# Kernel optimization log

Hardware: AMD Instinct MI355X
Metric: run time of the kernel (lower is better)

The kernel has to match this reference:

```python
import jax, jax.numpy as jnp
import numpy as np

N = 100000      # nodes
K = 16          # fixed degree (num_ngbrs)
E = N * K       # edges
NFEAT = 128
NHID = 64
OPFEAT = 64


def setup_inputs() -> dict:
    key = jax.random.key(0)
    ks = jax.random.split(key, 8)
    x = jax.random.normal(ks[0], (N, NFEAT), dtype=jnp.float32)
    # edges sorted by destination node, exactly K per node (required by the
    # original e.view(-1, num_ngbrs) softmax reshape)
    edge_row = jnp.repeat(jnp.arange(N, dtype=jnp.int32), K)
    edge_col = jax.random.randint(ks[1], (E,), 0, N, dtype=jnp.int32)
    stdv1 = 1.0 / np.sqrt(NHID)
    stdv2 = 1.0 / np.sqrt(OPFEAT)
    W1 = jax.random.uniform(ks[2], (NFEAT, NHID), jnp.float32, -stdv1, stdv1)
    b1 = jax.random.uniform(ks[3], (NHID,), jnp.float32, -stdv1, stdv1)
    a1 = jax.random.normal(ks[4], (2 * NHID,), jnp.float32) * 0.1
    W2 = jax.random.uniform(ks[5], (NHID, OPFEAT), jnp.float32, -stdv2, stdv2)
    b2 = jax.random.uniform(ks[6], (OPFEAT,), jnp.float32, -stdv2, stdv2)
    a2 = jax.random.normal(ks[7], (2 * OPFEAT,), jnp.float32) * 0.1
    return {"x": x, "edge_row": edge_row, "edge_col": edge_col,
            "W1": W1, "a1": a1, "b1": b1, "W2": W2, "a2": a2, "b2": b2,
            "k": K}


def _gat_layer(x, W, a, b, edge_row, edge_col, k):
    n = x.shape[0]
    h = x @ W                                        # [N, F_out]
    # edge score: concat(h[dst], h[src]) . a  -> leaky_relu
    h_edge = jnp.concatenate([h[edge_row], h[edge_col]], axis=1)  # [E, 2F]
    e = jax.nn.leaky_relu(h_edge @ a, negative_slope=0.2)         # [E]
    # per-destination softmax over the fixed K neighbors (edges row-sorted)
    att = jax.nn.softmax(e.reshape(-1, k), axis=1).reshape(-1)    # [E]
    att = jax.lax.stop_gradient(att)  # original detaches attention
    # sparse (adj * attention) @ h  ==  segment-sum of att_e * h[src_e]
    out = jax.ops.segment_sum(att[:, None] * h[edge_col], edge_row,
                              num_segments=n)
    return out + b


def reference(x, edge_row, edge_col, W1, a1, b1, W2, a2, b2, k):
    x1 = jax.nn.relu(_gat_layer(x, W1, a1, b1, edge_row, edge_col, k))
    x2 = jax.nn.relu(_gat_layer(x1, W2, a2, b2, edge_row, edge_col, k))
    return x2
```

## Files before the change

### kernel.cpp

```cpp
#include <hip/hip_runtime.h>


typedef __attribute__((ext_vector_type(8))) _Float16 f16x8;
typedef __attribute__((ext_vector_type(4))) _Float16 f16x4;
typedef __attribute__((ext_vector_type(4))) float floatx4;

__device__ inline float ubitf(unsigned u) { union { unsigned u; float f; } v; v.u = u; return v.f; }
__device__ inline unsigned fbitu(float f) { union { float f; unsigned u; } v; v.f = f; return v.u; }

template<int KD, bool A_F16>
__global__ __launch_bounds__(256, 2) void gemm_score_f16(
    const void* __restrict__ Xv, const float* __restrict__ W,
    const float* __restrict__ av, _Float16* __restrict__ H,
    float* __restrict__ s1, float* __restrict__ s2, int n)
{
    constexpr int NKT = KD / 32;
    constexpr int NF = NKT * 4 * 64;
    __shared__ f16x8 Bhi[NF];
    __shared__ f16x8 Blo[NF];
    const int tid = threadIdx.x;

    for (int f = tid; f < NF; f += 256) {
        const int ln = f & 63, ntk = f >> 6;
        const int kt = ntk >> 2, nt = ntk & 3;
        const int kbase = kt * 32 + (ln >> 4) * 8;
        const int ccol = nt * 16 + (ln & 15);
        f16x8 hh, ll;
#pragma unroll
        for (int j = 0; j < 8; j++) {
            const float w = W[(kbase + j) * 64 + ccol];
            const _Float16 wh = (_Float16)w;
            hh[j] = wh;
            ll[j] = (_Float16)(w - (float)wh);
        }
        Bhi[f] = hh; Blo[f] = ll;
    }
    __syncthreads();

    const int wave = tid >> 6, lane = tid & 63;
    const int quad = lane >> 4, l15 = lane & 15;
    const int r0 = blockIdx.x * 192 + wave * 48;

    float a1c[4], a2c[4];
#pragma unroll
    for (int nt = 0; nt < 4; nt++) {
        a1c[nt] = av[nt * 16 + l15];
        a2c[nt] = av[64 + nt * 16 + l15];
    }

    f16x8 A[NKT][3];
    if constexpr (A_F16) {
        const _Float16* X = (const _Float16*)Xv;
#pragma unroll
        for (int rb = 0; rb < 3; rb++) {
            int ra = r0 + rb * 16 + l15; if (ra > n - 1) ra = n - 1;
            const _Float16* xp = &X[(size_t)ra * KD + quad * 8];
#pragma unroll
            for (int kt = 0; kt < NKT; kt++)
                A[kt][rb] = *(const f16x8*)(xp + kt * 32);
        }
    } else {
        const float* X = (const float*)Xv;
        float4 raw[NKT][3][2];
#pragma unroll
        for (int rb = 0; rb < 3; rb++) {
            int ra = r0 + rb * 16 + l15; if (ra > n - 1) ra = n - 1;
            const float* xp = &X[(size_t)ra * KD + quad * 8];
#pragma unroll
            for (int kt = 0; kt < NKT; kt++) {
                raw[kt][rb][0] = *(const float4*)(xp + kt * 32);
                raw[kt][rb][1] = *(const float4*)(xp + kt * 32 + 4);
            }
        }
#pragma unroll
        for (int kt = 0; kt < NKT; kt++)
#pragma unroll
            for (int rb = 0; rb < 3; rb++) {
                f16x8 a;
                a[0] = (_Float16)raw[kt][rb][0].x; a[1] = (_Float16)raw[kt][rb][0].y;
                a[2] = (_Float16)raw[kt][rb][0].z; a[3] = (_Float16)raw[kt][rb][0].w;
                a[4] = (_Float16)raw[kt][rb][1].x; a[5] = (_Float16)raw[kt][rb][1].y;
                a[6] = (_Float16)raw[kt][rb][1].z; a[7] = (_Float16)raw[kt][rb][1].w;
                A[kt][rb] = a;
            }
    }

    floatx4 acc[4][3];
#pragma unroll
    for (int nt = 0; nt < 4; nt++)
#pragma unroll
        for (int rb = 0; rb < 3; rb++) acc[nt][rb] = (floatx4){0, 0, 0, 0};

#pragma unroll
    for (int kt = 0; kt < NKT; kt++) {
#pragma unroll
        for (int nt = 0; nt < 4; nt++) {
            const f16x8 bh = Bhi[(kt * 4 + nt) * 64 + lane];
            const f16x8 bl = Blo[(kt * 4 + nt) * 64 + lane];
#pragma unroll
            for (int rb = 0; rb < 3; rb++) {
                acc[nt][rb] = __builtin_amdgcn_mfma_f32_16x16x32_f16(A[kt][rb], bh, acc[nt][rb], 0, 0, 0);
                acc[nt][rb] = __builtin_amdgcn_mfma_f32_16x16x32_f16(A[kt][rb], bl, acc[nt][rb], 0, 0, 0);
            }
        }
    }

#pragma unroll
    for (int rb = 0; rb < 3; rb++) {
        float p1[4] = {0, 0, 0, 0}, p2[4] = {0, 0, 0, 0};
#pragma unroll
        for (int nt = 0; nt < 4; nt++) {
#pragma unroll
            for (int reg = 0; reg < 4; reg++) {
                const int r = r0 + rb * 16 + quad * 4 + reg;
                if (r < n) H[(size_t)r * 64 + nt * 16 + l15] = (_Float16)acc[nt][rb][reg];
                p1[reg] = fmaf(acc[nt][rb][reg], a1c[nt], p1[reg]);
                p2[reg] = fmaf(acc[nt][rb][reg], a2c[nt], p2[reg]);
            }
        }
#pragma unroll
        for (int m = 1; m < 16; m <<= 1) {
#pragma unroll
            for (int reg = 0; reg < 4; reg++) {
                p1[reg] += __shfl_xor(p1[reg], m, 64);
                p2[reg] += __shfl_xor(p2[reg], m, 64);
            }
        }
        if (l15 == 0) {
#pragma unroll
            for (int reg = 0; reg < 4; reg++) {
                const int r = r0 + rb * 16 + quad * 4 + reg;
                if (r < n) { s1[r] = p1[reg]; s2[r] = p2[reg]; }
            }
        }
    }
}

template<typename OT>
__global__ __launch_bounds__(512) void attn_agg(
    const _Float16* __restrict__ H, const float* __restrict__ s1,
    const float* __restrict__ s2, const int* __restrict__ col,
    const float* __restrict__ bias, OT* __restrict__ out, int n)
{
    const int lane = threadIdx.x & 63;
    const int wv = threadIdx.x >> 6;
    const int j = lane & 15;
    const int dst = blockIdx.x * 32 + wv * 4 + (lane >> 4);
    if (dst >= n) return;

    const int c = col[dst * 16 + j];
    float e = s1[dst] + s2[c];
    e = (e > 0.0f) ? e : 0.2f * e;
    float m = e;
#pragma unroll
    for (int mk = 1; mk < 16; mk <<= 1) m = fmaxf(m, __shfl_xor(m, mk, 64));
    float p = __expf(e - m);
    float s = p;
#pragma unroll
    for (int mk = 1; mk < 16; mk <<= 1) s += __shfl_xor(s, mk, 64);
    const float att = p / s;

    const int bbase = (lane & 48) << 2;
    int srck[16]; float attk[16];
#pragma unroll
    for (int k = 0; k < 16; k++) {
        const int bidx = bbase + (k << 2);
        srck[k] = __builtin_amdgcn_ds_bpermute(bidx, c);
        attk[k] = ubitf((unsigned)__builtin_amdgcn_ds_bpermute(bidx, (int)fbitu(att)));
    }
    f16x4 hv[16];
#pragma unroll
    for (int k = 0; k < 16; k++)
        hv[k] = *(const f16x4*)&H[(size_t)srck[k] * 64 + j * 4];

    float a0 = 0, a1 = 0, a2 = 0, a3 = 0;
#pragma unroll
    for (int k = 0; k < 16; k++) {
        a0 = fmaf(attk[k], (float)hv[k][0], a0);
        a1 = fmaf(attk[k], (float)hv[k][1], a1);
        a2 = fmaf(attk[k], (float)hv[k][2], a2);
        a3 = fmaf(attk[k], (float)hv[k][3], a3);
    }
    const float4 bv = *(const float4*)&bias[j * 4];
    const float o0 = fmaxf(a0 + bv.x, 0.0f);
    const float o1 = fmaxf(a1 + bv.y, 0.0f);
    const float o2 = fmaxf(a2 + bv.z, 0.0f);
    const float o3 = fmaxf(a3 + bv.w, 0.0f);
    if constexpr (sizeof(OT) == 2) {
        f16x4 o; o[0] = (_Float16)o0; o[1] = (_Float16)o1;
                 o[2] = (_Float16)o2; o[3] = (_Float16)o3;
        *(f16x4*)&out[(size_t)dst * 64 + j * 4] = o;
    } else {
        float4 o; o.x = o0; o.y = o1; o.z = o2; o.w = o3;
        *(float4*)&out[(size_t)dst * 64 + j * 4] = o;
    }
}

extern "C" void kernel_launch(void* const* d_in, const int* in_sizes, int n_in,
                              void* d_out, int out_size, void* d_ws, size_t ws_size,
                              hipStream_t stream)
{
    const float* x        = (const float*)d_in[0];
    const int*   edge_col = (const int*)  d_in[2];
    const float* W1       = (const float*)d_in[3];
    const float* a1       = (const float*)d_in[4];
    const float* b1       = (const float*)d_in[5];
    const float* W2       = (const float*)d_in[6];
    const float* a2       = (const float*)d_in[7];
    const float* b2       = (const float*)d_in[8];
    const int n = in_sizes[0] / 128;

    _Float16* h  = (_Float16*)d_ws;
    _Float16* xm = h + (size_t)n * 64;
    float* s1 = (float*)(xm + (size_t)n * 64);
    float* s2 = s1 + n;

    const int gemm_blocks = (n + 191) / 192;
    const int agg_blocks  = (n + 31) / 32;

    gemm_score_f16<128, false><<<gemm_blocks, 256, 0, stream>>>(x, W1, a1, h, s1, s2, n);
    attn_agg<_Float16><<<agg_blocks, 512, 0, stream>>>(h, s1, s2, edge_col, b1, xm, n);
    gemm_score_f16<64, true><<<gemm_blocks, 256, 0, stream>>>(xm, W2, a2, h, s1, s2, n);
    attn_agg<float><<<agg_blocks, 512, 0, stream>>>(h, s1, s2, edge_col, b2, (float*)d_out, n);
}
```

Before: 187.9 us.

## Fuse layer-1 attention aggregation with layer-2 GEMM and widen gather lanes

Merges the first attention/aggregation kernel with the second GEMM+score kernel. The aggregated hidden rows are staged in LDS instead of being written to and re-read from global memory, which also drops one launch. Both aggregation paths now use 8 lanes per destination, each gathering 16-byte f16x8 chunks instead of 8-byte ones. The fused kernel runs the gather at 256 threads with 48 rows per wave sequentially, so gather parallelism and occupancy may be lower than in the standalone kernel.

New measurement: 189.3 us. Within noise of the previous version (+0.8%).

```diff
diff --git a/kernel.cpp b/kernel.cpp
--- a/kernel.cpp
+++ b/kernel.cpp
@@ -8,9 +8,9 @@
 __device__ inline float ubitf(unsigned u) { union { unsigned u; float f; } v; v.u = u; return v.f; }
 __device__ inline unsigned fbitu(float f) { union { float f; unsigned u; } v; v.f = f; return v.u; }
 
-template<int KD, bool A_F16>
+template<int KD>
 __global__ __launch_bounds__(256, 2) void gemm_score_f16(
-    const void* __restrict__ Xv, const float* __restrict__ W,
+    const float* __restrict__ X, const float* __restrict__ W,
     const float* __restrict__ av, _Float16* __restrict__ H,
     float* __restrict__ s1, float* __restrict__ s2, int n)
 {
@@ -48,42 +48,29 @@
         a2c[nt] = av[64 + nt * 16 + l15];
     }
 
+    float4 raw[NKT][3][2];
+#pragma unroll
+    for (int rb = 0; rb < 3; rb++) {
+        int ra = r0 + rb * 16 + l15; if (ra > n - 1) ra = n - 1;
+        const float* xp = &X[(size_t)ra * KD + quad * 8];
+#pragma unroll
+        for (int kt = 0; kt < NKT; kt++) {
+            raw[kt][rb][0] = *(const float4*)(xp + kt * 32);
+            raw[kt][rb][1] = *(const float4*)(xp + kt * 32 + 4);
+        }
+    }
     f16x8 A[NKT][3];
-    if constexpr (A_F16) {
-        const _Float16* X = (const _Float16*)Xv;
+#pragma unroll
+    for (int kt = 0; kt < NKT; kt++)
 #pragma unroll
         for (int rb = 0; rb < 3; rb++) {
-            int ra = r0 + rb * 16 + l15; if (ra > n - 1) ra = n - 1;
-            const _Float16* xp = &X[(size_t)ra * KD + quad * 8];
-#pragma unroll
-            for (int kt = 0; kt < NKT; kt++)
-                A[kt][rb] = *(const f16x8*)(xp + kt * 32);
-        }
-    } else {
-        const float* X = (const float*)Xv;
-        float4 raw[NKT][3][2];
-#pragma unroll
-        for (int rb = 0; rb < 3; rb++) {
-            int ra = r0 + rb * 16 + l15; if (ra > n - 1) ra = n - 1;
-            const float* xp = &X[(size_t)ra * KD + quad * 8];
-#pragma unroll
-            for (int kt = 0; kt < NKT; kt++) {
-                raw[kt][rb][0] = *(const float4*)(xp + kt * 32);
-                raw[kt][rb][1] = *(const float4*)(xp + kt * 32 + 4);
-            }
-        }
-#pragma unroll
-        for (int kt = 0; kt < NKT; kt++)
-#pragma unroll
-            for (int rb = 0; rb < 3; rb++) {
-                f16x8 a;
-                a[0] = (_Float16)raw[kt][rb][0].x; a[1] = (_Float16)raw[kt][rb][0].y;
-                a[2] = (_Float16)raw[kt][rb][0].z; a[3] = (_Float16)raw[kt][rb][0].w;
-                a[4] = (_Float16)raw[kt][rb][1].x; a[5] = (_Float16)raw[kt][rb][1].y;
-                a[6] = (_Float16)raw[kt][rb][1].z; a[7] = (_Float16)raw[kt][rb][1].w;
-                A[kt][rb] = a;
-            }
-    }
+            f16x8 a;
+            a[0] = (_Float16)raw[kt][rb][0].x; a[1] = (_Float16)raw[kt][rb][0].y;
+            a[2] = (_Float16)raw[kt][rb][0].z; a[3] = (_Float16)raw[kt][rb][0].w;
+            a[4] = (_Float16)raw[kt][rb][1].x; a[5] = (_Float16)raw[kt][rb][1].y;
+            a[6] = (_Float16)raw[kt][rb][1].z; a[7] = (_Float16)raw[kt][rb][1].w;
+            A[kt][rb] = a;
+        }
 
     floatx4 acc[4][3];
 #pragma unroll
@@ -92,7 +79,7 @@
         for (int rb = 0; rb < 3; rb++) acc[nt][rb] = (floatx4){0, 0, 0, 0};
 
 #pragma unroll
-    for (int kt = 0; kt < NKT; kt++) {
+    for (int kt = 0; kt < NKT; kt++)
 #pragma unroll
         for (int nt = 0; nt < 4; nt++) {
             const f16x8 bh = Bhi[(kt * 4 + nt) * 64 + lane];
@@ -103,13 +90,12 @@
                 acc[nt][rb] = __builtin_amdgcn_mfma_f32_16x16x32_f16(A[kt][rb], bl, acc[nt][rb], 0, 0, 0);
             }
         }
-    }
 
 #pragma unroll
     for (int rb = 0; rb < 3; rb++) {
         float p1[4] = {0, 0, 0, 0}, p2[4] = {0, 0, 0, 0};
 #pragma unroll
-        for (int nt = 0; nt < 4; nt++) {
+        for (int nt = 0; nt < 4; nt++)
 #pragma unroll
             for (int reg = 0; reg < 4; reg++) {
                 const int r = r0 + rb * 16 + quad * 4 + reg;
@@ -117,82 +103,234 @@
                 p1[reg] = fmaf(acc[nt][rb][reg], a1c[nt], p1[reg]);
                 p2[reg] = fmaf(acc[nt][rb][reg], a2c[nt], p2[reg]);
             }
-        }
-#pragma unroll
-        for (int m = 1; m < 16; m <<= 1) {
+#pragma unroll
+        for (int m = 1; m < 16; m <<= 1)
 #pragma unroll
             for (int reg = 0; reg < 4; reg++) {
                 p1[reg] += __shfl_xor(p1[reg], m, 64);
                 p2[reg] += __shfl_xor(p2[reg], m, 64);
             }
-        }
-        if (l15 == 0) {
+        if (l15 == 0)
 #pragma unroll
             for (int reg = 0; reg < 4; reg++) {
                 const int r = r0 + rb * 16 + quad * 4 + reg;
                 if (r < n) { s1[r] = p1[reg]; s2[r] = p2[reg]; }
             }
-        }
     }
 }
 
-template<typename OT>
-__global__ __launch_bounds__(512) void attn_agg(
+__global__ __launch_bounds__(256, 2) void attn_gemm_fused(
+    const _Float16* __restrict__ H1, const float* __restrict__ s1a,
+    const float* __restrict__ s2a, const int* __restrict__ col,
+    const float* __restrict__ bias1, const float* __restrict__ W2,
+    const float* __restrict__ av, _Float16* __restrict__ H2,
+    float* __restrict__ s1b, float* __restrict__ s2b, int n)
+{
+    constexpr int NKT = 2;
+    constexpr int NF = NKT * 4 * 64;
+    constexpr int XST = 72;
+    __shared__ f16x8 Bhi[NF];
+    __shared__ f16x8 Blo[NF];
+    __shared__ _Float16 Xs[4][48 * XST];
+    const int tid = threadIdx.x;
+
+    for (int f = tid; f < NF; f += 256) {
+        const int ln = f & 63, ntk = f >> 6;
+        const int kt = ntk >> 2, nt = ntk & 3;
+        const int kbase = kt * 32 + (ln >> 4) * 8;
+        const int ccol = nt * 16 + (ln & 15);
+        f16x8 hh, ll;
+#pragma unroll
+        for (int j = 0; j < 8; j++) {
+            const float w = W2[(kbase + j) * 64 + ccol];
+            const _Float16 wh = (_Float16)w;
+            hh[j] = wh;
+            ll[j] = (_Float16)(w - (float)wh);
+        }
+        Bhi[f] = hh; Blo[f] = ll;
+    }
+    __syncthreads();
+
+    const int wave = tid >> 6, lane = tid & 63;
+    const int g = (lane >> 3) & 7, j = lane & 7;
+    const int r0 = blockIdx.x * 192 + wave * 48;
+    _Float16* xw = Xs[wave];
+
+    float bb[8];
+    *(float4*)&bb[0] = *(const float4*)&bias1[j * 8];
+    *(float4*)&bb[4] = *(const float4*)&bias1[j * 8 + 4];
+
+    int c0v[6], c1v[6]; float s1v[6];
+#pragma unroll
+    for (int ch = 0; ch < 6; ch++) {
+        int dc = r0 + ch * 8 + g; if (dc > n - 1) dc = n - 1;
+        c0v[ch] = col[dc * 16 + j];
+        c1v[ch] = col[dc * 16 + 8 + j];
+        s1v[ch] = s1a[dc];
+    }
+    float e0v[6], e1v[6];
+#pragma unroll
+    for (int ch = 0; ch < 6; ch++) {
+        e0v[ch] = s1v[ch] + s2a[c0v[ch]];
+        e1v[ch] = s1v[ch] + s2a[c1v[ch]];
+    }
+    const int bb4 = (lane & 56) << 2;
+#pragma unroll
+    for (int ch = 0; ch < 6; ch++) {
+        float e0 = e0v[ch]; e0 = (e0 > 0.0f) ? e0 : 0.2f * e0;
+        float e1 = e1v[ch]; e1 = (e1 > 0.0f) ? e1 : 0.2f * e1;
+        float m = fmaxf(e0, e1);
+        m = fmaxf(m, __shfl_xor(m, 1, 64));
+        m = fmaxf(m, __shfl_xor(m, 2, 64));
+        m = fmaxf(m, __shfl_xor(m, 4, 64));
+        const float p0 = __expf(e0 - m), p1 = __expf(e1 - m);
+        float s = p0 + p1;
+        s += __shfl_xor(s, 1, 64); s += __shfl_xor(s, 2, 64); s += __shfl_xor(s, 4, 64);
+        const float inv = 1.0f / s;
+        const float att0 = p0 * inv, att1 = p1 * inv;
+
+        int srck[16]; float attk[16];
+#pragma unroll
+        for (int k = 0; k < 8; k++) {
+            srck[k]     = __builtin_amdgcn_ds_bpermute(bb4 + 4 * k, c0v[ch]);
+            srck[k + 8] = __builtin_amdgcn_ds_bpermute(bb4 + 4 * k, c1v[ch]);
+            attk[k]     = ubitf((unsigned)__builtin_amdgcn_ds_bpermute(bb4 + 4 * k, (int)fbitu(att0)));
+            attk[k + 8] = ubitf((unsigned)__builtin_amdgcn_ds_bpermute(bb4 + 4 * k, (int)fbitu(att1)));
+        }
+        f16x8 hv[16];
+#pragma unroll
+        for (int k = 0; k < 16; k++)
+            hv[k] = *(const f16x8*)&H1[(size_t)srck[k] * 64 + j * 8];
+        float acc[8] = {0, 0, 0, 0, 0, 0, 0, 0};
+#pragma unroll
+        for (int k = 0; k < 16; k++)
+#pragma unroll
+            for (int t = 0; t < 8; t++)
+                acc[t] = fmaf(attk[k], (float)hv[k][t], acc[t]);
+        f16x8 xv;
+#pragma unroll
+        for (int t = 0; t < 8; t++)
+            xv[t] = (_Float16)fmaxf(acc[t] + bb[t], 0.0f);
+        *(f16x8*)&xw[(ch * 8 + g) * XST + j * 8] = xv;
+    }
+
+    const int quad = lane >> 4, l15 = lane & 15;
+    float a1c[4], a2c[4];
+#pragma unroll
+    for (int nt = 0; nt < 4; nt++) {
+        a1c[nt] = av[nt * 16 + l15];
+        a2c[nt] = av[64 + nt * 16 + l15];
+    }
+    floatx4 acc2[4][3];
+#pragma unroll
+    for (int nt = 0; nt < 4; nt++)
+#pragma unroll
+        for (int rb = 0; rb < 3; rb++) acc2[nt][rb] = (floatx4){0, 0, 0, 0};
+
+#pragma unroll
+    for (int kt = 0; kt < NKT; kt++) {
+        f16x8 A[3];
+#pragma unroll
+        for (int rb = 0; rb < 3; rb++)
+            A[rb] = *(const f16x8*)&xw[(rb * 16 + l15) * XST + kt * 32 + quad * 8];
+#pragma unroll
+        for (int nt = 0; nt < 4; nt++) {
+            const f16x8 bh = Bhi[(kt * 4 + nt) * 64 + lane];
+            const f16x8 bl = Blo[(kt * 4 + nt) * 64 + lane];
+#pragma unroll
+            for (int rb = 0; rb < 3; rb++) {
+                acc2[nt][rb] = __builtin_amdgcn_mfma_f32_16x16x32_f16(A[rb], bh, acc2[nt][rb], 0, 0, 0);
+                acc2[nt][rb] = __builtin_amdgcn_mfma_f32_16x16x32_f16(A[rb], bl, acc2[nt][rb], 0, 0, 0);
+            }
+        }
+    }
+
+#pragma unroll
+    for (int rb = 0; rb < 3; rb++) {
+        float p1[4] = {0, 0, 0, 0}, p2[4] = {0, 0, 0, 0};
+#pragma unroll
+        for (int nt = 0; nt < 4; nt++)
+#pragma unroll
+            for (int reg = 0; reg < 4; reg++) {
+                const int r = r0 + rb * 16 + quad * 4 + reg;
+                if (r < n) H2[(size_t)r * 64 + nt * 16 + l15] = (_Float16)acc2[nt][rb][reg];
+                p1[reg] = fmaf(acc2[nt][rb][reg], a1c[nt], p1[reg]);
+                p2[reg] = fmaf(acc2[nt][rb][reg], a2c[nt], p2[reg]);
+            }
+#pragma unroll
+        for (int m = 1; m < 16; m <<= 1)
+#pragma unroll
+            for (int reg = 0; reg < 4; reg++) {
+                p1[reg] += __shfl_xor(p1[reg], m, 64);
+                p2[reg] += __shfl_xor(p2[reg], m, 64);
+            }
+        if (l15 == 0)
+#pragma unroll
+            for (int reg = 0; reg < 4; reg++) {
+                const int r = r0 + rb * 16 + quad * 4 + reg;
+                if (r < n) { s1b[r] = p1[reg]; s2b[r] = p2[reg]; }
+            }
+    }
+}
+
+__global__ __launch_bounds__(512) void attn_final(
     const _Float16* __restrict__ H, const float* __restrict__ s1,
     const float* __restrict__ s2, const int* __restrict__ col,
-    const float* __restrict__ bias, OT* __restrict__ out, int n)
+    const float* __restrict__ bias, float* __restrict__ out, int n)
 {
     const int lane = threadIdx.x & 63;
     const int wv = threadIdx.x >> 6;
-    const int j = lane & 15;
-    const int dst = blockIdx.x * 32 + wv * 4 + (lane >> 4);
-    if (dst >= n) return;
-
-    const int c = col[dst * 16 + j];
-    float e = s1[dst] + s2[c];
-    e = (e > 0.0f) ? e : 0.2f * e;
-    float m = e;
-#pragma unroll
-    for (int mk = 1; mk < 16; mk <<= 1) m = fmaxf(m, __shfl_xor(m, mk, 64));
-    float p = __expf(e - m);
-    float s = p;
-#pragma unroll
-    for (int mk = 1; mk < 16; mk <<= 1) s += __shfl_xor(s, mk, 64);
-    const float att = p / s;
-
-    const int bbase = (lane & 48) << 2;
+    const int g = (lane >> 3) & 7, j = lane & 7;
+    const int dst = blockIdx.x * 64 + wv * 8 + g;
+    const int dc = (dst > n - 1) ? (n - 1) : dst;
+
+    const int c0 = col[dc * 16 + j];
+    const int c1 = col[dc * 16 + 8 + j];
+    const float s1d = s1[dc];
+    float e0 = s1d + s2[c0];
+    float e1 = s1d + s2[c1];
+    e0 = (e0 > 0.0f) ? e0 : 0.2f * e0;
+    e1 = (e1 > 0.0f) ? e1 : 0.2f * e1;
+    float m = fmaxf(e0, e1);
+    m = fmaxf(m, __shfl_xor(m, 1, 64));
+    m = fmaxf(m, __shfl_xor(m, 2, 64));
+    m = fmaxf(m, __shfl_xor(m, 4, 64));
+    const float p0 = __expf(e0 - m), p1 = __expf(e1 - m);
+    float s = p0 + p1;
+    s += __shfl_xor(s, 1, 64); s += __shfl_xor(s, 2, 64); s += __shfl_xor(s, 4, 64);
+    const float inv = 1.0f / s;
+    const float att0 = p0 * inv, att1 = p1 * inv;
+
+    const int bb4 = (lane & 56) << 2;
     int srck[16]; float attk[16];
 #pragma unroll
-    for (int k = 0; k < 16; k++) {
-        const int bidx = bbase + (k << 2);
-        srck[k] = __builtin_amdgcn_ds_bpermute(bidx, c);
-        attk[k] = ubitf((unsigned)__builtin_amdgcn_ds_bpermute(bidx, (int)fbitu(att)));
-    }
-    f16x4 hv[16];
+    for (int k = 0; k < 8; k++) {
+        srck[k]     = __builtin_amdgcn_ds_bpermute(bb4 + 4 * k, c0);
+        srck[k + 8] = __builtin_amdgcn_ds_bpermute(bb4 + 4 * k, c1);
+        attk[k]     = ubitf((unsigned)__builtin_amdgcn_ds_bpermute(bb4 + 4 * k, (int)fbitu(att0)));
+        attk[k + 8] = ubitf((unsigned)__builtin_amdgcn_ds_bpermute(bb4 + 4 * k, (int)fbitu(att1)));
+    }
+    f16x8 hv[16];
 #pragma unroll
     for (int k = 0; k < 16; k++)
-        hv[k] = *(const f16x4*)&H[(size_t)srck[k] * 64 + j * 4];
-
-    float a0 = 0, a1 = 0, a2 = 0, a3 = 0;
-#pragma unroll
-    for (int k = 0; k < 16; k++) {
-        a0 = fmaf(attk[k], (float)hv[k][0], a0);
-        a1 = fmaf(attk[k], (float)hv[k][1], a1);
-        a2 = fmaf(attk[k], (float)hv[k][2], a2);
-        a3 = fmaf(attk[k], (float)hv[k][3], a3);
-    }
-    const float4 bv = *(const float4*)&bias[j * 4];
-    const float o0 = fmaxf(a0 + bv.x, 0.0f);
-    const float o1 = fmaxf(a1 + bv.y, 0.0f);
-    const float o2 = fmaxf(a2 + bv.z, 0.0f);
-    const float o3 = fmaxf(a3 + bv.w, 0.0f);
-    if constexpr (sizeof(OT) == 2) {
-        f16x4 o; o[0] = (_Float16)o0; o[1] = (_Float16)o1;
-                 o[2] = (_Float16)o2; o[3] = (_Float16)o3;
-        *(f16x4*)&out[(size_t)dst * 64 + j * 4] = o;
-    } else {
-        float4 o; o.x = o0; o.y = o1; o.z = o2; o.w = o3;
-        *(float4*)&out[(size_t)dst * 64 + j * 4] = o;
+        hv[k] = *(const f16x8*)&H[(size_t)srck[k] * 64 + j * 8];
+    float acc[8] = {0, 0, 0, 0, 0, 0, 0, 0};
+#pragma unroll
+    for (int k = 0; k < 16; k++)
+#pragma unroll
+        for (int t = 0; t < 8; t++)
+            acc[t] = fmaf(attk[k], (float)hv[k][t], acc[t]);
+
+    if (dst < n) {
+        float4 b0 = *(const float4*)&bias[j * 8];
+        float4 b1v = *(const float4*)&bias[j * 8 + 4];
+        float4 o0, o1;
+        o0.x = fmaxf(acc[0] + b0.x, 0.0f); o0.y = fmaxf(acc[1] + b0.y, 0.0f);
+        o0.z = fmaxf(acc[2] + b0.z, 0.0f); o0.w = fmaxf(acc[3] + b0.w, 0.0f);
+        o1.x = fmaxf(acc[4] + b1v.x, 0.0f); o1.y = fmaxf(acc[5] + b1v.y, 0.0f);
+        o1.z = fmaxf(acc[6] + b1v.z, 0.0f); o1.w = fmaxf(acc[7] + b1v.w, 0.0f);
+        *(float4*)&out[(size_t)dst * 64 + j * 8] = o0;
+        *(float4*)&out[(size_t)dst * 64 + j * 8 + 4] = o1;
     }
 }
 
@@ -210,16 +348,18 @@
     const float* b2       = (const float*)d_in[8];
     const int n = in_sizes[0] / 128;
 
-    _Float16* h  = (_Float16*)d_ws;
-    _Float16* xm = h + (size_t)n * 64;
-    float* s1 = (float*)(xm + (size_t)n * 64);
-    float* s2 = s1 + n;
+    _Float16* h1 = (_Float16*)d_ws;
+    _Float16* h2 = h1 + (size_t)n * 64;
+    float* s1a = (float*)(h2 + (size_t)n * 64);
+    float* s2a = s1a + n;
+    float* s1b = s2a + n;
+    float* s2b = s1b + n;
 
     const int gemm_blocks = (n + 191) / 192;
-    const int agg_blocks  = (n + 31) / 32;
-
-    gemm_score_f16<128, false><<<gemm_blocks, 256, 0, stream>>>(x, W1, a1, h, s1, s2, n);
-    attn_agg<_Float16><<<agg_blocks, 512, 0, stream>>>(h, s1, s2, edge_col, b1, xm, n);
-    gemm_score_f16<64, true><<<gemm_blocks, 256, 0, stream>>>(xm, W2, a2, h, s1, s2, n);
-    attn_agg<float><<<agg_blocks, 512, 0, stream>>>(h, s1, s2, edge_col, b2, (float*)d_out, n);
+    const int fin_blocks  = (n + 63) / 64;
+
+    gemm_score_f16<128><<<gemm_blocks, 256, 0, stream>>>(x, W1, a1, h1, s1a, s2a, n);
+    attn_gemm_fused<<<gemm_blocks, 256, 0, stream>>>(h1, s1a, s2a, edge_col, b1,
+                                                     W2, a2, h2, s1b, s2b, n);
+    attn_final<<<fin_blocks, 512, 0, stream>>>(h2, s1b, s2b, edge_col, b2, (float*)d_out, n);
 }
```
